# Performance work log

Hardware: AMD Instinct MI355X
Metric: run time of the kernel (lower is better)

## Reference

```python
import jax, jax.numpy as jnp
import numpy as np

S, B, D, F, E, K = 1024, 2, 512, 2048, 8, 2


def setup_inputs() -> dict:
    key = jax.random.key(0)
    ks = jax.random.split(key, 12)
    s = lambda *sh: 1.0 / np.sqrt(sh[0])
    inp = {
        "x": jax.random.normal(ks[0], (S, B, D), dtype=jnp.float32),
        # gate: nn.Linear(d_model, n_experts)
        "Wg": jax.random.normal(ks[1], (D, E), dtype=jnp.float32) * s(D),
        "bg": jnp.zeros((E,), dtype=jnp.float32),
        # routed experts: stacked FFN params (E copies of expert)
        "W1": jax.random.normal(ks[2], (E, D, F), dtype=jnp.float32) * s(D),
        "b1": jnp.zeros((E, F), dtype=jnp.float32),
        "W2": jax.random.normal(ks[3], (E, F, D), dtype=jnp.float32) * s(F),
        "b2": jnp.zeros((E, D), dtype=jnp.float32),
        # shared expert (single FFN)
        "Ws1": jax.random.normal(ks[4], (D, F), dtype=jnp.float32) * s(D),
        "bs1": jnp.zeros((F,), dtype=jnp.float32),
        "Ws2": jax.random.normal(ks[5], (F, D), dtype=jnp.float32) * s(F),
        "bs2": jnp.zeros((D,), dtype=jnp.float32),
    }
    return inp


def reference(x, Wg, bg, W1, b1, W2, b2, Ws1, bs1, Ws2, bs2):
    # gate_logits: (S, B, E)
    gate_logits = jnp.einsum("sbd,de->sbe", x, Wg) + bg
    # top-k per token (eval mode: k = n_experts_per_token, t = 1.0)
    weights, selected = jax.lax.top_k(gate_logits, K)  # (S,B,K)
    weights = jax.nn.softmax(weights.astype(jnp.float32), axis=-1)
    # combine weights per expert: (S,B,E)
    onehot = jax.nn.one_hot(selected, E, dtype=weights.dtype)  # (S,B,K,E)
    comb = jnp.einsum("sbk,sbke->sbe", weights, onehot)
    # routed experts computed densely, combined with per-token routing weight
    h = jax.nn.relu(jnp.einsum("sbd,edf->sbef", x, W1) + b1)  # (S,B,E,F)
    y = jnp.einsum("sbef,efd->sbed", h, W2) + b2              # (S,B,E,D)
    out = jnp.einsum("sbe,sbed->sbd", comb, y)
    # shared expert, scaled by 1/k
    hs = jax.nn.relu(jnp.einsum("sbd,df->sbf", x, Ws1) + bs1)
    shared = jnp.einsum("sbf,fd->sbd", hs, Ws2) + bs2
    out = out + (1.0 / K) * shared
    return out
```

## Files before the change

kernel.cpp:

```cpp
#include <hip/hip_runtime.h>
#include <hip/hip_bf16.h>
#include <stdint.h>

#define TT 2048
#define DD 512
#define FF 2048
#define EE 8

typedef unsigned short u16;
typedef __attribute__((ext_vector_type(8))) unsigned short ushort8v;
typedef __attribute__((ext_vector_type(8))) short short8;
typedef __attribute__((ext_vector_type(4))) float float4v;

__device__ __forceinline__ u16 f2bf(float f) {
    unsigned u = __float_as_uint(f);
    u += 0x7FFF + ((u >> 16) & 1);
    return (u16)(u >> 16);
}

__device__ __forceinline__ void gl_lds16(const u16* g, u16* l) {
    __builtin_amdgcn_global_load_lds(
        (const __attribute__((address_space(1))) unsigned int*)g,
        (__attribute__((address_space(3))) unsigned int*)l, 16, 0, 0);
}

#define WS_HB   0ull
#define WS_XG   (WS_HB + 6144ull*2048*2)
#define WS_WT1  (WS_XG + 2048ull*512*2)
#define WS_ME   (WS_WT1 + 9ull*2048*512*2)
#define WS_MW   (WS_ME + 16384)
#define WS_RT   (WS_MW + 16384)
#define WS_WROW (WS_RT + 16384)
#define WS_RTG  (WS_WROW + 16384)
#define WS_WT2  (WS_RTG + 128)
#define WS_NEED (WS_WT2 + 9ull*2048*512*2)

__device__ __forceinline__ void conv_unit(int j, const float* __restrict__ srcE,
                                          const float* __restrict__ srcS,
                                          u16* __restrict__ dst,
                                          int R, int C, int shC, u16* Ls) {
    int mid = j >> 8, t2 = j & 255;
    int tr = t2 >> shC, tc = t2 & ((1 << shC) - 1);
    int r0 = tr * 64, c0 = tc * 64;
    const float* src = (mid < 8) ? srcE + (size_t)mid * R * C : srcS;
    u16* dstm = dst + (size_t)mid * R * C;
    int t = threadIdx.x;
#pragma unroll
    for (int i = 0; i < 4; ++i) {
        int rr = (t >> 4) + i * 16;
        int cc = (t & 15) * 4;
        float4v v = *(const float4v*)(src + (size_t)(r0 + rr) * C + c0 + cc);
#pragma unroll
        for (int jx = 0; jx < 4; ++jx) Ls[(cc + jx) * 72 + rr] = f2bf(v[jx]);
    }
    __syncthreads();
#pragma unroll
    for (int jj = 0; jj < 2; ++jj) {
        int slot = t + jj * 256;
        int cc = slot >> 3, r8 = (slot & 7) * 8;
        ushort8v o = *(const ushort8v*)&Ls[cc * 72 + r8];
        *(ushort8v*)(dstm + (size_t)(c0 + cc) * R + r0 + r8) = o;
    }
}

__device__ __forceinline__ void gate_wave(int t, int lane,
                                          const float* __restrict__ x,
                                          const float* __restrict__ Wg,
                                          const float* __restrict__ bg,
                                          int* __restrict__ metaE,
                                          float* __restrict__ metaW,
                                          u16* __restrict__ xg) {
    const float* xp = x + (size_t)t * DD + lane * 8;
    float4v x0 = *(const float4v*)xp;
    float4v x1 = *(const float4v*)(xp + 4);
    float xf[8] = {x0[0], x0[1], x0[2], x0[3], x1[0], x1[1], x1[2], x1[3]};
    float acc[EE] = {0.f, 0.f, 0.f, 0.f, 0.f, 0.f, 0.f, 0.f};
#pragma unroll
    for (int g = 0; g < 8; ++g) {
        const float* wp = Wg + (size_t)(lane * 8 + g) * EE;
        float4v w0 = *(const float4v*)wp;
        float4v w1 = *(const float4v*)(wp + 4);
        acc[0] += xf[g] * w0[0]; acc[1] += xf[g] * w0[1];
        acc[2] += xf[g] * w0[2]; acc[3] += xf[g] * w0[3];
        acc[4] += xf[g] * w1[0]; acc[5] += xf[g] * w1[1];
        acc[6] += xf[g] * w1[2]; acc[7] += xf[g] * w1[3];
    }
#pragma unroll
    for (int off = 1; off < 64; off <<= 1) {
#pragma unroll
        for (int e = 0; e < EE; ++e) acc[e] += __shfl_xor(acc[e], off, 64);
    }
    ushort8v xv;
#pragma unroll
    for (int jx = 0; jx < 4; ++jx) xv[jx] = f2bf(x0[jx]);
#pragma unroll
    for (int jx = 0; jx < 4; ++jx) xv[4 + jx] = f2bf(x1[jx]);
    *(ushort8v*)(xg + (size_t)t * DD + lane * 8) = xv;
    if (lane == 0) {
#pragma unroll
        for (int e = 0; e < EE; ++e) acc[e] += bg[e];
        int e0 = 0; float l0 = acc[0];
#pragma unroll
        for (int e = 1; e < EE; ++e) if (acc[e] > l0) { l0 = acc[e]; e0 = e; }
        int e1 = -1; float l1 = -3.4e38f;
#pragma unroll
        for (int e = 0; e < EE; ++e)
            if (e != e0 && acc[e] > l1) { l1 = acc[e]; e1 = e; }
        float ex = __expf(l1 - l0);
        float w0 = 1.f / (1.f + ex);
        metaE[2 * t] = e0; metaE[2 * t + 1] = e1;
        metaW[2 * t] = w0; metaW[2 * t + 1] = 1.f - w0;
    }
}

__global__ __launch_bounds__(256) void fused1_k(
    const float* __restrict__ x, const float* __restrict__ Wg,
    const float* __restrict__ bg,
    const float* __restrict__ W1, const float* __restrict__ Ws1,
    const float* __restrict__ W2, const float* __restrict__ Ws2,
    float* __restrict__ out, u16* __restrict__ xg,
    u16* __restrict__ Wt1, u16* __restrict__ Wt2,
    int* __restrict__ metaE, float* __restrict__ metaW, int nconv) {
    __shared__ __align__(16) u16 Ls[64 * 72];
    int b = blockIdx.x, tid = threadIdx.x;
    if (b < nconv) {
        if (b < 2304) conv_unit(b, W1, Ws1, Wt1, DD, FF, 5, Ls);
        else          conv_unit(b - 2304, W2, Ws2, Wt2, FF, DD, 3, Ls);
    } else if (b < nconv + 512) {
        int gb = b - nconv;
        gate_wave(gb * 4 + (tid >> 6), tid & 63, x, Wg, bg, metaE, metaW, xg);
    } else {
        int zb = b - nconv - 512;
        float* op = out + (size_t)zb * 8192;
#pragma unroll
        for (int it = 0; it < 8; ++it)
            *(float4v*)(op + it * 1024 + tid * 4) = (float4v){0.f, 0.f, 0.f, 0.f};
    }
}

__global__ __launch_bounds__(256) void conv2_k(const float* __restrict__ W2,
                                               const float* __restrict__ Ws2,
                                               u16* __restrict__ Wt2) {
    __shared__ __align__(16) u16 Ls[64 * 72];
    conv_unit(blockIdx.x, W2, Ws2, Wt2, FF, DD, 3, Ls);
}

__global__ __launch_bounds__(256) void rank_k(const int* __restrict__ metaE,
                                              const float* __restrict__ metaW,
                                              int* __restrict__ routing,
                                              int* __restrict__ rtok,
                                              float* __restrict__ wrow) {
    __shared__ __align__(16) char smem[16384];
    u16* er      = (u16*)smem;
    int* segCnt  = (int*)(smem + 8192);
    int* segBase = (int*)(smem + 10240);
    int* expTot  = (int*)(smem + 12288);
    int tid = threadIdx.x, wv = tid >> 6, lane = tid & 63;
    unsigned long long below = (lane == 0) ? 0ull : ((~0ull) >> (64 - lane));
    for (int s = wv * 16; s < wv * 16 + 16; ++s) {
        int entry = s * 64 + lane;
        int e = metaE[entry];
        int rk = 0;
#pragma unroll
        for (int ee = 0; ee < 8; ++ee) {
            unsigned long long m = __ballot(e == ee);
            if (e == ee) rk = __popcll(m & below);
            if (lane == ee) segCnt[s * 8 + ee] = __popcll(m);
        }
        er[entry] = (u16)(e | (rk << 4));
    }
    __syncthreads();
    if (tid < 8) {
        int s = 0;
        for (int g = 0; g < 64; ++g) { segBase[g * 8 + tid] = s; s += segCnt[g * 8 + tid]; }
        expTot[tid] = s;
    }
    __syncthreads();
    if (tid == 0) {
        int s = 0;
        for (int e = 0; e < 8; ++e) { int c = expTot[e]; expTot[8 + e] = s; s += c; }
    }
    __syncthreads();
    if (tid < 8) { routing[tid] = expTot[8 + tid]; routing[8 + tid] = expTot[tid]; }
    for (int i = 0; i < 16; ++i) {
        int entry = tid + i * 256;
        int v = er[entry];
        int e = v & 15, rk = v >> 4;
        int row = expTot[8 + e] + segBase[(entry >> 6) * 8 + e] + rk;
        rtok[row] = entry >> 1;
        wrow[row] = metaW[entry];
    }
}

__global__ __launch_bounds__(256) void gemmA_k(
    const u16* __restrict__ xg, const u16* __restrict__ Wt1,
    const float* __restrict__ b1, const float* __restrict__ bs1,
    const int* __restrict__ routing, const int* __restrict__ rtok,
    u16* __restrict__ hbuf) {
    __shared__ __align__(16) u16 As[2][64 * 64];
    __shared__ __align__(16) u16 Bs[2][128 * 64];
    const int* offs = routing; const int* cnt = routing + 8;
    int j = blockIdx.x, tid = threadIdx.x;
    int rt, ct, Mloc, hRowBase, rowBase; bool routed;
    const u16* Bsrc; const float* bias;
    if (j < 512) {
        rt = j >> 4; ct = j & 15; Mloc = 64; rowBase = rt * 64;
        Bsrc = Wt1 + (size_t)8 * FF * DD; bias = bs1;
        hRowBase = 4096 + rt * 64; routed = false;
    } else {
        int jr = j - 512; int e = jr & 7; int rc = jr >> 3;
        rt = rc >> 4; ct = rc & 15;
        int M = cnt[e]; if (rt * 64 >= M) return;
        Mloc = M - rt * 64; if (Mloc > 64) Mloc = 64;
        rowBase = offs[e] + rt * 64;
        Bsrc = Wt1 + (size_t)e * FF * DD; bias = b1 + e * FF;
        hRowBase = rowBase; routed = true;
    }
    int n0 = ct * 128;
    int lane = tid & 63, w = tid >> 6, ln = lane & 15, quad = lane >> 4;
    int lr8 = lane >> 3;
    int cs = (lane & 7) ^ lr8;
    const u16* ApS[2];
#pragma unroll
    for (int i = 0; i < 2; ++i) {
        int r = w * 16 + i * 8 + lr8;
        int tok;
        if (routed) { int br = rowBase + r; if (br > 4095) br = 4095; tok = rtok[br]; }
        else tok = rowBase + r;
        ApS[i] = xg + (size_t)tok * DD + cs * 8;
    }
    const u16* BpS[4];
#pragma unroll
    for (int i = 0; i < 4; ++i) {
        int r = w * 32 + i * 8 + lr8;
        BpS[i] = Bsrc + (size_t)(n0 + r) * DD + cs * 8;
    }
    float4v acc[2][4];
#pragma unroll
    for (int a = 0; a < 2; ++a)
#pragma unroll
        for (int b = 0; b < 4; ++b) acc[a][b] = (float4v){0.f, 0.f, 0.f, 0.f};

    auto stage = [&](int kt, int pb) {
        u16* Ab = &As[pb][0]; u16* Bb = &Bs[pb][0];
#pragma unroll
        for (int i = 0; i < 2; ++i)
            gl_lds16(ApS[i] + kt * 64, Ab + (w * 16 + i * 8) * 64);
#pragma unroll
        for (int i = 0; i < 4; ++i)
            gl_lds16(BpS[i] + kt * 64, Bb + (w * 32 + i * 8) * 64);
    };

    stage(0, 0);
#pragma unroll
    for (int kt = 0; kt < 8; ++kt) {
        int pb = kt & 1;
        if (kt < 7) {
            stage(kt + 1, pb ^ 1);
            asm volatile("s_waitcnt vmcnt(6)" ::: "memory");
        } else {
            asm volatile("s_waitcnt vmcnt(0)" ::: "memory");
        }
        __builtin_amdgcn_s_barrier();
        __builtin_amdgcn_sched_barrier(0);
        const u16* Ab = &As[pb][0]; const u16* Bb = &Bs[pb][0];
#pragma unroll
        for (int s = 0; s < 2; ++s) {
            int chs = ((s * 4 + quad) ^ (ln & 7)) * 8;
            short8 Af[2], Bf[4];
#pragma unroll
            for (int a = 0; a < 2; ++a) {
                int ra = (w & 1) * 32 + a * 16 + ln;
                Af[a] = *(const short8*)(Ab + ra * 64 + chs);
            }
#pragma unroll
            for (int b = 0; b < 4; ++b) {
                int rb = (w >> 1) * 64 + b * 16 + ln;
                Bf[b] = *(const short8*)(Bb + rb * 64 + chs);
            }
#pragma unroll
            for (int a = 0; a < 2; ++a)
#pragma unroll
                for (int b = 0; b < 4; ++b)
                    acc[a][b] = __builtin_amdgcn_mfma_f32_16x16x32_bf16(Af[a], Bf[b], acc[a][b], 0, 0, 0);
        }
        __builtin_amdgcn_sched_barrier(0);
        __builtin_amdgcn_s_barrier();
    }
#pragma unroll
    for (int b = 0; b < 4; ++b) {
        int n = n0 + (w >> 1) * 64 + b * 16 + ln;
        float bv = bias[n];
#pragma unroll
        for (int a = 0; a < 2; ++a) {
#pragma unroll
            for (int i = 0; i < 4; ++i) {
                int lr = (w & 1) * 32 + a * 16 + quad * 4 + i;
                if (lr < Mloc) {
                    float v = acc[a][b][i] + bv;
                    v = v > 0.f ? v : 0.f;
                    hbuf[(size_t)(hRowBase + lr) * FF + n] = f2bf(v);
                }
            }
        }
    }
}

__global__ __launch_bounds__(256) void gemmB_k(
    const u16* __restrict__ hbuf, const u16* __restrict__ Wt2,
    const float* __restrict__ b2, const float* __restrict__ bs2,
    const int* __restrict__ routing, const int* __restrict__ rtok,
    const float* __restrict__ wrow, float* __restrict__ out) {
    __shared__ __align__(16) u16 As[2][64 * 64];
    __shared__ __align__(16) u16 Bs[2][128 * 64];
    const int* offs = routing; const int* cnt = routing + 8;
    int j = blockIdx.x, tid = threadIdx.x;
    int rt, ct, ks, Mloc, aRowBase; bool sh;
    const u16* Bsrc; const float* bias;
    if (j < 256) {
        sh = true; rt = j >> 3; int sub = j & 7; ct = sub >> 1; ks = sub & 1;
        Mloc = 64; aRowBase = 4096 + rt * 64;
        Bsrc = Wt2 + (size_t)8 * DD * FF; bias = bs2;
    } else {
        sh = false; int jr = j - 256; int e = jr & 7; int rc = jr >> 3;
        rt = rc >> 3; ct = (rc >> 1) & 3; ks = rc & 1;
        int M = cnt[e]; if (rt * 64 >= M) return;
        Mloc = M - rt * 64; if (Mloc > 64) Mloc = 64;
        aRowBase = offs[e] + rt * 64;
        Bsrc = Wt2 + (size_t)e * DD * FF; bias = b2 + e * DD;
    }
    int n0 = ct * 128;
    int lane = tid & 63, w = tid >> 6, ln = lane & 15, quad = lane >> 4;
    int lr8 = lane >> 3;
    int cs = (lane & 7) ^ lr8;
    const u16* ApS[2];
#pragma unroll
    for (int i = 0; i < 2; ++i) {
        int r = w * 16 + i * 8 + lr8;
        ApS[i] = hbuf + (size_t)(aRowBase + r) * FF + ks * 1024 + cs * 8;
    }
    const u16* BpS[4];
#pragma unroll
    for (int i = 0; i < 4; ++i) {
        int r = w * 32 + i * 8 + lr8;
        BpS[i] = Bsrc + (size_t)(n0 + r) * FF + ks * 1024 + cs * 8;
    }
    float4v acc[2][4];
#pragma unroll
    for (int a = 0; a < 2; ++a)
#pragma unroll
        for (int b = 0; b < 4; ++b) acc[a][b] = (float4v){0.f, 0.f, 0.f, 0.f};

    auto stage = [&](int kt, int pb) {
        u16* Ab = &As[pb][0]; u16* Bb = &Bs[pb][0];
#pragma unroll
        for (int i = 0; i < 2; ++i)
            gl_lds16(ApS[i] + kt * 64, Ab + (w * 16 + i * 8) * 64);
#pragma unroll
        for (int i = 0; i < 4; ++i)
            gl_lds16(BpS[i] + kt * 64, Bb + (w * 32 + i * 8) * 64);
    };

    stage(0, 0);
#pragma unroll
    for (int kt = 0; kt < 16; ++kt) {
        int pb = kt & 1;
        if (kt < 15) {
            stage(kt + 1, pb ^ 1);
            asm volatile("s_waitcnt vmcnt(6)" ::: "memory");
        } else {
            asm volatile("s_waitcnt vmcnt(0)" ::: "memory");
        }
        __builtin_amdgcn_s_barrier();
        __builtin_amdgcn_sched_barrier(0);
        const u16* Ab = &As[pb][0]; const u16* Bb = &Bs[pb][0];
#pragma unroll
        for (int s = 0; s < 2; ++s) {
            int chs = ((s * 4 + quad) ^ (ln & 7)) * 8;
            short8 Af[2], Bf[4];
#pragma unroll
            for (int a = 0; a < 2; ++a) {
                int ra = (w & 1) * 32 + a * 16 + ln;
                Af[a] = *(const short8*)(Ab + ra * 64 + chs);
            }
#pragma unroll
            for (int b = 0; b < 4; ++b) {
                int rb = (w >> 1) * 64 + b * 16 + ln;
                Bf[b] = *(const short8*)(Bb + rb * 64 + chs);
            }
#pragma unroll
            for (int a = 0; a < 2; ++a)
#pragma unroll
                for (int b = 0; b < 4; ++b)
                    acc[a][b] = __builtin_amdgcn_mfma_f32_16x16x32_bf16(Af[a], Bf[b], acc[a][b], 0, 0, 0);
        }
        __builtin_amdgcn_sched_barrier(0);
        __builtin_amdgcn_s_barrier();
    }
    float bv[4];
#pragma unroll
    for (int b = 0; b < 4; ++b)
        bv[b] = (ks == 0) ? bias[n0 + (w >> 1) * 64 + b * 16 + ln] : 0.f;
#pragma unroll
    for (int a = 0; a < 2; ++a) {
#pragma unroll
        for (int i = 0; i < 4; ++i) {
            int lr = (w & 1) * 32 + a * 16 + quad * 4 + i;
            if (lr < Mloc) {
                int row = aRowBase + lr;
                int t; float wr;
                if (sh) { t = row - 4096; wr = 0.5f; }
                else    { t = rtok[row]; wr = wrow[row]; }
                float* op = out + (size_t)t * DD;
#pragma unroll
                for (int b = 0; b < 4; ++b) {
                    int n = n0 + (w >> 1) * 64 + b * 16 + ln;
                    atomicAdd(op + n, wr * (acc[a][b][i] + bv[b]));
                }
            }
        }
    }
}

extern "C" void kernel_launch(void* const* d_in, const int* in_sizes, int n_in,
                              void* d_out, int out_size, void* d_ws, size_t ws_size,
                              hipStream_t stream) {
    const float* x   = (const float*)d_in[0];
    const float* Wg  = (const float*)d_in[1];
    const float* bg  = (const float*)d_in[2];
    const float* W1  = (const float*)d_in[3];
    const float* b1  = (const float*)d_in[4];
    const float* W2  = (const float*)d_in[5];
    const float* b2  = (const float*)d_in[6];
    const float* Ws1 = (const float*)d_in[7];
    const float* bs1 = (const float*)d_in[8];
    const float* Ws2 = (const float*)d_in[9];
    const float* bs2 = (const float*)d_in[10];
    float* out = (float*)d_out;

    char* ws = (char*)d_ws;
    u16*   hbuf    = (u16*)(ws + WS_HB);
    u16*   xg      = (u16*)(ws + WS_XG);
    u16*   Wt1     = (u16*)(ws + WS_WT1);
    int*   metaE   = (int*)(ws + WS_ME);
    float* metaW   = (float*)(ws + WS_MW);
    int*   rtok    = (int*)(ws + WS_RT);
    float* wrow    = (float*)(ws + WS_WROW);
    int*   routing = (int*)(ws + WS_RTG);
    bool   big     = ws_size >= WS_NEED;
    u16*   Wt2     = big ? (u16*)(ws + WS_WT2) : Wt1;
    int    nconv   = big ? 4608 : 2304;

    fused1_k<<<nconv + 640, 256, 0, stream>>>(x, Wg, bg, W1, Ws1, W2, Ws2,
                                              out, xg, Wt1, Wt2, metaE, metaW, nconv);
    rank_k<<<1, 256, 0, stream>>>(metaE, metaW, routing, rtok, wrow);
    gemmA_k<<<8704, 256, 0, stream>>>(xg, Wt1, b1, bs1, routing, rtok, hbuf);
    if (!big) conv2_k<<<2304, 256, 0, stream>>>(W2, Ws2, Wt2);
    gemmB_k<<<4352, 256, 0, stream>>>(hbuf, Wt2, b2, bs2, routing, rtok, wrow, out);
}
```

Baseline: 220.7 us.

## Replace atomic split-K down-projection with full-K GEMM plus gather combine

In the large-workspace path, the down-projection GEMM now runs the full K=2048 with 512-thread blocks (8 waves on a 64x128 tile) instead of split-K. It writes unweighted per-row expert outputs to a float scratch buffer that reuses the Wt1 region. A new combine kernel then gathers each token's two routed rows and its shared row through a token-to-row map produced by rank_k. This removes the need to zero the output in fused1 (fewer blocks there) and the atomic or accumulate writes into out, at the cost of an extra kernel launch and a round trip of the intermediate through memory.

```diff
diff --git a/kernel.cpp b/kernel.cpp
--- a/kernel.cpp
+++ b/kernel.cpp
@@ -31,7 +31,8 @@
 #define WS_MW   (WS_ME + 16384)
 #define WS_RT   (WS_MW + 16384)
 #define WS_WROW (WS_RT + 16384)
-#define WS_RTG  (WS_WROW + 16384)
+#define WS_TROW (WS_WROW + 16384)
+#define WS_RTG  (WS_TROW + 16384)
 #define WS_WT2  (WS_RTG + 128)
 #define WS_NEED (WS_WT2 + 9ull*2048*512*2)
 
@@ -149,7 +150,8 @@
                                               const float* __restrict__ metaW,
                                               int* __restrict__ routing,
                                               int* __restrict__ rtok,
-                                              float* __restrict__ wrow) {
+                                              float* __restrict__ wrow,
+                                              int* __restrict__ trow) {
     __shared__ __align__(16) char smem[16384];
     u16* er      = (u16*)smem;
     int* segCnt  = (int*)(smem + 8192);
@@ -189,6 +191,7 @@
         int row = expTot[8 + e] + segBase[(entry >> 6) * 8 + e] + rk;
         rtok[row] = entry >> 1;
         wrow[row] = metaW[entry];
+        trow[entry] = row;
     }
 }
 
@@ -306,7 +309,121 @@
     }
 }
 
-__global__ __launch_bounds__(256) void gemmB_k(
+__global__ __launch_bounds__(512) void gemmB_k(
+    const u16* __restrict__ hbuf, const u16* __restrict__ Wt2,
+    const float* __restrict__ b2, const float* __restrict__ bs2,
+    const int* __restrict__ routing, float* __restrict__ ybuf) {
+    __shared__ __align__(16) u16 As[2][64 * 64];
+    __shared__ __align__(16) u16 Bs[2][128 * 64];
+    const int* offs = routing; const int* cnt = routing + 8;
+    int j = blockIdx.x, tid = threadIdx.x;
+    int rt, ct, Mloc, aRowBase;
+    const u16* Bsrc; const float* bias;
+    if (j < 128) {
+        rt = j >> 2; ct = j & 3;
+        Mloc = 64; aRowBase = 4096 + rt * 64;
+        Bsrc = Wt2 + (size_t)8 * DD * FF; bias = bs2;
+    } else {
+        int jr = j - 128; int e = jr & 7; int rc = jr >> 3;
+        rt = rc >> 2; ct = rc & 3;
+        int M = cnt[e]; if (rt * 64 >= M) return;
+        Mloc = M - rt * 64; if (Mloc > 64) Mloc = 64;
+        aRowBase = offs[e] + rt * 64;
+        Bsrc = Wt2 + (size_t)e * DD * FF; bias = b2 + e * DD;
+    }
+    int n0 = ct * 128;
+    int lane = tid & 63, w = tid >> 6, ln = lane & 15, quad = lane >> 4;
+    int wm = w >> 2, wn = w & 3;
+    int lr8 = lane >> 3;
+    int cs = (lane & 7) ^ lr8;
+    const u16* ApS = hbuf + (size_t)(aRowBase + w * 8 + lr8) * FF + cs * 8;
+    const u16* BpS[2];
+#pragma unroll
+    for (int i = 0; i < 2; ++i)
+        BpS[i] = Bsrc + (size_t)(n0 + w * 16 + i * 8 + lr8) * FF + cs * 8;
+    float4v acc[2][2];
+#pragma unroll
+    for (int a = 0; a < 2; ++a)
+#pragma unroll
+        for (int b = 0; b < 2; ++b) acc[a][b] = (float4v){0.f, 0.f, 0.f, 0.f};
+
+    auto stage = [&](int kt, int pb) {
+        gl_lds16(ApS + kt * 64, &As[pb][0] + (w * 8) * 64);
+#pragma unroll
+        for (int i = 0; i < 2; ++i)
+            gl_lds16(BpS[i] + kt * 64, &Bs[pb][0] + (w * 16 + i * 8) * 64);
+    };
+
+    stage(0, 0);
+#pragma unroll
+    for (int kt = 0; kt < 32; ++kt) {
+        int pb = kt & 1;
+        if (kt < 31) {
+            stage(kt + 1, pb ^ 1);
+            asm volatile("s_waitcnt vmcnt(3)" ::: "memory");
+        } else {
+            asm volatile("s_waitcnt vmcnt(0)" ::: "memory");
+        }
+        __builtin_amdgcn_s_barrier();
+        __builtin_amdgcn_sched_barrier(0);
+        const u16* Ab = &As[pb][0]; const u16* Bb = &Bs[pb][0];
+#pragma unroll
+        for (int s = 0; s < 2; ++s) {
+            int chs = ((s * 4 + quad) ^ (ln & 7)) * 8;
+            short8 Af[2], Bf[2];
+#pragma unroll
+            for (int a = 0; a < 2; ++a) {
+                int ra = wm * 32 + a * 16 + ln;
+                Af[a] = *(const short8*)(Ab + ra * 64 + chs);
+            }
+#pragma unroll
+            for (int b = 0; b < 2; ++b) {
+                int rb = wn * 32 + b * 16 + ln;
+                Bf[b] = *(const short8*)(Bb + rb * 64 + chs);
+            }
+#pragma unroll
+            for (int a = 0; a < 2; ++a)
+#pragma unroll
+                for (int b = 0; b < 2; ++b)
+                    acc[a][b] = __builtin_amdgcn_mfma_f32_16x16x32_bf16(Af[a], Bf[b], acc[a][b], 0, 0, 0);
+        }
+        __builtin_amdgcn_sched_barrier(0);
+        __builtin_amdgcn_s_barrier();
+    }
+#pragma unroll
+    for (int b = 0; b < 2; ++b) {
+        int n = n0 + wn * 32 + b * 16 + ln;
+        float bv = bias[n];
+#pragma unroll
+        for (int a = 0; a < 2; ++a) {
+#pragma unroll
+            for (int i = 0; i < 4; ++i) {
+                int lr = wm * 32 + a * 16 + quad * 4 + i;
+                if (lr < Mloc)
+                    ybuf[(size_t)(aRowBase + lr) * DD + n] = acc[a][b][i] + bv;
+            }
+        }
+    }
+}
+
+__global__ __launch_bounds__(256) void combine_k(
+    const float* __restrict__ ybuf, const int* __restrict__ trow,
+    const float* __restrict__ metaW, float* __restrict__ out) {
+    int tid = threadIdx.x;
+    int tok = blockIdx.x * 2 + (tid >> 7);
+    int q = (tid & 127) * 4;
+    int r0 = trow[2 * tok], r1 = trow[2 * tok + 1];
+    float w0 = metaW[2 * tok], w1 = metaW[2 * tok + 1];
+    float4v y0 = *(const float4v*)(ybuf + (size_t)r0 * DD + q);
+    float4v y1 = *(const float4v*)(ybuf + (size_t)r1 * DD + q);
+    float4v ys = *(const float4v*)(ybuf + (size_t)(4096 + tok) * DD + q);
+    float4v o;
+#pragma unroll
+    for (int i = 0; i < 4; ++i) o[i] = w0 * y0[i] + w1 * y1[i] + 0.5f * ys[i];
+    *(float4v*)(out + (size_t)tok * DD + q) = o;
+}
+
+__global__ __launch_bounds__(256) void gemmBat_k(
     const u16* __restrict__ hbuf, const u16* __restrict__ Wt2,
     const float* __restrict__ b2, const float* __restrict__ bs2,
     const int* __restrict__ routing, const int* __restrict__ rtok,
@@ -350,7 +467,6 @@
     for (int a = 0; a < 2; ++a)
 #pragma unroll
         for (int b = 0; b < 4; ++b) acc[a][b] = (float4v){0.f, 0.f, 0.f, 0.f};
-
     auto stage = [&](int kt, int pb) {
         u16* Ab = &As[pb][0]; u16* Bb = &Bs[pb][0];
 #pragma unroll
@@ -360,7 +476,6 @@
         for (int i = 0; i < 4; ++i)
             gl_lds16(BpS[i] + kt * 64, Bb + (w * 32 + i * 8) * 64);
     };
-
     stage(0, 0);
 #pragma unroll
     for (int kt = 0; kt < 16; ++kt) {
@@ -446,15 +561,23 @@
     float* metaW   = (float*)(ws + WS_MW);
     int*   rtok    = (int*)(ws + WS_RT);
     float* wrow    = (float*)(ws + WS_WROW);
+    int*   trow    = (int*)(ws + WS_TROW);
     int*   routing = (int*)(ws + WS_RTG);
     bool   big     = ws_size >= WS_NEED;
     u16*   Wt2     = big ? (u16*)(ws + WS_WT2) : Wt1;
+    float* ybuf    = (float*)(ws + WS_WT1);
     int    nconv   = big ? 4608 : 2304;
-
-    fused1_k<<<nconv + 640, 256, 0, stream>>>(x, Wg, bg, W1, Ws1, W2, Ws2,
-                                              out, xg, Wt1, Wt2, metaE, metaW, nconv);
-    rank_k<<<1, 256, 0, stream>>>(metaE, metaW, routing, rtok, wrow);
+    int    ngrid1  = big ? (nconv + 512) : (nconv + 640);
+
+    fused1_k<<<ngrid1, 256, 0, stream>>>(x, Wg, bg, W1, Ws1, W2, Ws2,
+                                         out, xg, Wt1, Wt2, metaE, metaW, nconv);
+    rank_k<<<1, 256, 0, stream>>>(metaE, metaW, routing, rtok, wrow, trow);
     gemmA_k<<<8704, 256, 0, stream>>>(xg, Wt1, b1, bs1, routing, rtok, hbuf);
-    if (!big) conv2_k<<<2304, 256, 0, stream>>>(W2, Ws2, Wt2);
-    gemmB_k<<<4352, 256, 0, stream>>>(hbuf, Wt2, b2, bs2, routing, rtok, wrow, out);
-}
+    if (big) {
+        gemmB_k<<<2176, 512, 0, stream>>>(hbuf, Wt2, b2, bs2, routing, ybuf);
+        combine_k<<<1024, 256, 0, stream>>>(ybuf, trow, metaW, out);
+    } else {
+        conv2_k<<<2304, 256, 0, stream>>>(W2, Ws2, Wt2);
+        gemmBat_k<<<4352, 256, 0, stream>>>(hbuf, Wt2, b2, bs2, routing, rtok, wrow, out);
+    }
+}
```

New measurement: 209.1 us. -5.3%, faster.
